# Optimization experiments

Measured on AMD Instinct MI355X. Metric: run time of the kernel, lower is better.

The kernel has to match this reference:

```python
import jax, jax.numpy as jnp
import numpy as np

N_NODES = 100000
N_EDGES = 1600000
DIM = 128


def setup_inputs() -> dict:
    key = jax.random.key(0)
    k1, k2, k3, k4 = jax.random.split(key, 4)
    x = jax.random.normal(k1, (N_NODES, DIM), dtype=jnp.float32)
    edge_index = jax.random.randint(k2, (2, N_EDGES), 0, N_NODES, dtype=jnp.int64)
    # PyG GCNConv params: Linear weight [out, in] (glorot) and bias [out] (zeros -> use small randn for a non-trivial grad path)
    W = jax.random.normal(k3, (DIM, DIM), dtype=jnp.float32) * (1.0 / np.sqrt(DIM))
    b = jax.random.normal(k4, (DIM,), dtype=jnp.float32) * 0.01
    return {"x": x, "edge_index": edge_index, "W": W, "b": b}


def reference(x, edge_index, W, b):
    # Faithful GCNConv: add self-loops, symmetric deg^-1/2 normalization,
    # linear transform, scatter-add aggregation, bias.
    N = x.shape[0]
    loop = jnp.arange(N, dtype=edge_index.dtype)
    src = jnp.concatenate([edge_index[0], loop])  # [E+N]
    dst = jnp.concatenate([edge_index[1], loop])  # [E+N]

    # degree (with self-loops) on destination nodes
    deg = jax.ops.segment_sum(jnp.ones_like(dst, dtype=x.dtype), dst, num_segments=N)
    dinv = jnp.where(deg > 0, jax.lax.rsqrt(deg), 0.0)
    norm = dinv[src] * dinv[dst]  # [E+N]

    x_lin = x @ W.T  # [N, dim] — PyG applies linear before propagate
    msg = x_lin[src] * norm[:, None]  # [E+N, dim] gather + scale
    out = jax.ops.segment_sum(msg, dst, num_segments=N)  # scatter-add aggregate
    return out + b
```

## Files before the change

kernel.cpp:

```cpp
#include <hip/hip_runtime.h>
#include <hip/hip_bf16.h>


#define DIM 128
#define BINSHIFT 9
#define BINSZ 512
#define MAXNB 256
#define WSTRIDE 136
#define SCAT_BLOCKS 256

typedef __attribute__((ext_vector_type(8))) short short8;
typedef __attribute__((ext_vector_type(4))) float f32x4;

__device__ inline unsigned short f2bf(float f) {
    unsigned u = __builtin_bit_cast(unsigned, f);
    return (unsigned short)((u + 0x7FFFu + ((u >> 16) & 1u)) >> 16);
}

__device__ inline void bf8_axpy(uint4 v, float s, float* acc) {
    acc[0] = fmaf(s, __builtin_bit_cast(float, v.x << 16), acc[0]);
    acc[1] = fmaf(s, __builtin_bit_cast(float, v.x & 0xFFFF0000u), acc[1]);
    acc[2] = fmaf(s, __builtin_bit_cast(float, v.y << 16), acc[2]);
    acc[3] = fmaf(s, __builtin_bit_cast(float, v.y & 0xFFFF0000u), acc[3]);
    acc[4] = fmaf(s, __builtin_bit_cast(float, v.z << 16), acc[4]);
    acc[5] = fmaf(s, __builtin_bit_cast(float, v.z & 0xFFFF0000u), acc[5]);
    acc[6] = fmaf(s, __builtin_bit_cast(float, v.w << 16), acc[6]);
    acc[7] = fmaf(s, __builtin_bit_cast(float, v.w & 0xFFFF0000u), acc[7]);
}


__global__ __launch_bounds__(256) void bin_hist(const int* __restrict__ dst, int E,
                                                int* __restrict__ hist, int nb) {
    __shared__ int lh[MAXNB];
    int t = threadIdx.x;
    lh[t] = 0;
    __syncthreads();
    int chunk = (E + gridDim.x - 1) / gridDim.x;
    int base = blockIdx.x * chunk, end = min(E, base + chunk);
    for (int i = base + t; i < end; i += 256)
        atomicAdd(&lh[dst[i] >> BINSHIFT], 1);
    __syncthreads();
    if (t < nb && lh[t]) atomicAdd(&hist[t], lh[t]);
}

__global__ __launch_bounds__(256) void bin_scan(const int* __restrict__ hist,
                                                int* __restrict__ binStart,
                                                int* __restrict__ binCursor,
                                                int* __restrict__ row_ptr,
                                                int nb, int N) {
    __shared__ int sa[MAXNB], sb[MAXNB];
    int t = threadIdx.x;
    sa[t] = (t < nb) ? hist[t] : 0;
    __syncthreads();
    int* src = sa; int* dstp = sb;
    for (int step = 1; step < MAXNB; step <<= 1) {
        int v = src[t];
        if (t >= step) v += src[t - step];
        dstp[t] = v;
        __syncthreads();
        int* tmp = src; src = dstp; dstp = tmp;
    }
    if (t < nb) {
        int excl = src[t] - hist[t];
        binStart[t] = excl;
        binCursor[t] = excl;
    }
    if (t == nb - 1) binStart[nb] = src[t];
    if (t == 0) row_ptr[N] = src[nb - 1];
}

__global__ __launch_bounds__(256) void csr_build(const int2* __restrict__ binned,
                                                 const int* __restrict__ binStart,
                                                 int* __restrict__ col,
                                                 int* __restrict__ row_ptr,
                                                 float* __restrict__ dinv, int N) {
    __shared__ int ldeg[BINSZ];
    __shared__ int sa[BINSZ], sb[BINSZ];
    __shared__ int lcur[BINSZ];
    int t = threadIdx.x, b = blockIdx.x;
    int s0 = binStart[b], s1 = binStart[b + 1];
    for (int i = t; i < BINSZ; i += 256) { ldeg[i] = 0; lcur[i] = 0; }
    __syncthreads();
    for (int i = s0 + t; i < s1; i += 256)
        atomicAdd(&ldeg[binned[i].y & (BINSZ - 1)], 1);
    __syncthreads();
    for (int i = t; i < BINSZ; i += 256) sa[i] = ldeg[i];
    __syncthreads();
    int* src = sa; int* dstp = sb;
    for (int step = 1; step < BINSZ; step <<= 1) {
        for (int i = t; i < BINSZ; i += 256) {
            int v = src[i];
            if (i >= step) v += src[i - step];
            dstp[i] = v;
        }
        __syncthreads();
        int* tmp = src; src = dstp; dstp = tmp;
    }
    for (int i = t; i < BINSZ; i += 256) dstp[i] = src[i] - ldeg[i];
    __syncthreads();
    for (int i = t; i < BINSZ; i += 256) {
        int n = (b << BINSHIFT) + i;
        if (n < N) {
            row_ptr[n] = s0 + dstp[i];
            dinv[n] = rsqrtf((float)(ldeg[i] + 1));
        }
    }
    for (int i = s0 + t; i < s1; i += 256) {
        int2 e = binned[i];
        int li = e.y & (BINSZ - 1);
        col[s0 + dstp[li] + atomicAdd(&lcur[li], 1)] = e.x;
    }
}


__global__ __launch_bounds__(256) void gemm_scatter(const float* __restrict__ x,
                                                    const float* __restrict__ W,
                                                    unsigned short* __restrict__ xlin, int N,
                                                    const int* __restrict__ ei, int E,
                                                    int* __restrict__ binCursor,
                                                    int2* __restrict__ binned, int nb) {
    __shared__ unsigned short wbf[DIM * WSTRIDE];
    __shared__ unsigned short obuf[4 * 16 * WSTRIDE];
    int t = threadIdx.x;

    if (blockIdx.x < SCAT_BLOCKS) {
        int* lh = (int*)wbf;
        int* lbase = lh + MAXNB;
        lh[t] = 0;
        __syncthreads();
        int chunk = (E + SCAT_BLOCKS - 1) / SCAT_BLOCKS;
        int base = blockIdx.x * chunk, end = min(E, base + chunk);
        for (int i = base + t; i < end; i += 256)
            atomicAdd(&lh[ei[E + i] >> BINSHIFT], 1);
        __syncthreads();
        if (t < nb) {
            int c = lh[t];
            lbase[t] = c ? atomicAdd(&binCursor[t], c) : 0;
            lh[t] = 0;
        }
        __syncthreads();
        for (int i = base + t; i < end; i += 256) {
            int s = ei[i], d = ei[E + i];
            int b = d >> BINSHIFT;
            int pos = lbase[b] + atomicAdd(&lh[b], 1);
            binned[pos] = make_int2(s, d);
        }
        return;
    }

    for (int it = 0; it < 16; ++it) {
        int f = it * 256 + t;
        int j = f >> 5;
        int kq = f & 31;
        float4 w4 = ((const float4*)W)[f];
        unsigned short* p = &wbf[j * WSTRIDE + kq * 4];
        p[0] = f2bf(w4.x); p[1] = f2bf(w4.y); p[2] = f2bf(w4.z); p[3] = f2bf(w4.w);
    }
    __syncthreads();

    int wid = t >> 6, lane = t & 63;
    int m = lane & 15, quad = lane >> 4;
    int row_base = (blockIdx.x - SCAT_BLOCKS) * 64 + wid * 16;

    f32x4 acc[8];
#pragma unroll
    for (int j = 0; j < 8; ++j) acc[j] = (f32x4){0.f, 0.f, 0.f, 0.f};

    int arow = row_base + m;
    if (arow >= N) arow = N - 1;
    const float* xr = x + (size_t)arow * DIM + quad * 8;

#pragma unroll
    for (int kc = 0; kc < 4; ++kc) {
        float4 a0 = *(const float4*)(xr + kc * 32);
        float4 a1 = *(const float4*)(xr + kc * 32 + 4);
        short8 af;
        af[0] = (short)f2bf(a0.x); af[1] = (short)f2bf(a0.y);
        af[2] = (short)f2bf(a0.z); af[3] = (short)f2bf(a0.w);
        af[4] = (short)f2bf(a1.x); af[5] = (short)f2bf(a1.y);
        af[6] = (short)f2bf(a1.z); af[7] = (short)f2bf(a1.w);
#pragma unroll
        for (int jt = 0; jt < 8; ++jt) {
            short8 bf = *(const short8*)&wbf[(jt * 16 + m) * WSTRIDE + kc * 32 + quad * 8];
            acc[jt] = __builtin_amdgcn_mfma_f32_16x16x32_bf16(af, bf, acc[jt], 0, 0, 0);
        }
    }

    unsigned short* ob = &obuf[wid * 16 * WSTRIDE];
#pragma unroll
    for (int jt = 0; jt < 8; ++jt)
#pragma unroll
        for (int r = 0; r < 4; ++r)
            ob[(quad * 4 + r) * WSTRIDE + jt * 16 + m] = f2bf(acc[jt][r]);
#pragma unroll
    for (int it = 0; it < 4; ++it) {
        int idx = it * 64 + lane;
        int r = idx >> 4;
        int cb = idx & 15;
        int grow = row_base + r;
        if (grow < N) {
            short8 v = *(const short8*)&ob[r * WSTRIDE + cb * 8];
            *(short8*)(xlin + (size_t)grow * DIM + cb * 8) = v;
        }
    }
}


__global__ __launch_bounds__(256) void aggregate(const unsigned short* __restrict__ xlin,
                                                 const int* __restrict__ col,
                                                 const int* __restrict__ row_ptr,
                                                 const float* __restrict__ dinv,
                                                 const float* __restrict__ bias,
                                                 float* __restrict__ out, int N) {
    int node = blockIdx.x * 16 + (threadIdx.x >> 4);
    int lane = threadIdx.x & 15;
    if (node >= N) return;

    float di = dinv[node];
    int r0 = row_ptr[node], r1 = row_ptr[node + 1];

    const uint4* xl = (const uint4*)xlin;
    float acc[8] = {};
    bf8_axpy(xl[(size_t)node * 16 + lane], di, acc);

    int i = r0;
    for (; i + 4 <= r1; i += 4) {
        int s0 = col[i], s1 = col[i + 1], s2 = col[i + 2], s3 = col[i + 3];
        float d0 = dinv[s0], d1 = dinv[s1], d2 = dinv[s2], d3 = dinv[s3];
        uint4 v0 = xl[(size_t)s0 * 16 + lane];
        uint4 v1 = xl[(size_t)s1 * 16 + lane];
        uint4 v2 = xl[(size_t)s2 * 16 + lane];
        uint4 v3 = xl[(size_t)s3 * 16 + lane];
        bf8_axpy(v0, d0, acc);
        bf8_axpy(v1, d1, acc);
        bf8_axpy(v2, d2, acc);
        bf8_axpy(v3, d3, acc);
    }
    for (; i < r1; ++i) {
        int s = col[i];
        bf8_axpy(xl[(size_t)s * 16 + lane], dinv[s], acc);
    }

    const float4* b4 = (const float4*)(bias + lane * 8);
    float4 bl = b4[0], bh = b4[1];
    float4 olo = make_float4(di * acc[0] + bl.x, di * acc[1] + bl.y,
                             di * acc[2] + bl.z, di * acc[3] + bl.w);
    float4 ohi = make_float4(di * acc[4] + bh.x, di * acc[5] + bh.y,
                             di * acc[6] + bh.z, di * acc[7] + bh.w);
    float4* op = (float4*)(out + (size_t)node * DIM + lane * 8);
    op[0] = olo;
    op[1] = ohi;
}


extern "C" void kernel_launch(void* const* d_in, const int* in_sizes, int n_in,
                              void* d_out, int out_size, void* d_ws, size_t ws_size,
                              hipStream_t stream) {
    const float* x    = (const float*)d_in[0];
    const int*   ei   = (const int*)d_in[1];
    const float* W    = (const float*)d_in[2];
    const float* bias = (const float*)d_in[3];
    float* out = (float*)d_out;

    const int N = in_sizes[0] / DIM;
    const int E = in_sizes[1] / 2;
    const int nb = (N + BINSZ - 1) >> BINSHIFT;

    char* ws = (char*)d_ws;
    size_t off = 0;
    auto alloc = [&](size_t bytes) { size_t o = off; off = (off + bytes + 255) & ~(size_t)255; return o; };
    unsigned short* xlin = (unsigned short*)(ws + alloc((size_t)N * DIM * 2));
    int2* binned   = (int2*) (ws + alloc((size_t)E * 8));
    int*  col      = (int*)  (ws + alloc((size_t)E * 4));
    int*  row_ptr  = (int*)  (ws + alloc((size_t)(N + 1) * 4));
    float* dinv    = (float*)(ws + alloc((size_t)N * 4));
    int*  hist     = (int*)  (ws + alloc(MAXNB * 4));
    int*  binStart = (int*)  (ws + alloc((MAXNB + 1) * 4));
    int*  binCursor= (int*)  (ws + alloc(MAXNB * 4));

    hipMemsetAsync(hist, 0, MAXNB * 4, stream);
    bin_hist<<<256, 256, 0, stream>>>(ei + E, E, hist, nb);
    bin_scan<<<1, MAXNB, 0, stream>>>(hist, binStart, binCursor, row_ptr, nb, N);
    gemm_scatter<<<SCAT_BLOCKS + (N + 63) / 64, 256, 0, stream>>>(
        x, W, xlin, N, ei, E, binCursor, binned, nb);
    csr_build<<<nb, 256, 0, stream>>>(binned, binStart, col, row_ptr, dinv, N);
    aggregate<<<(N + 15) / 16, 256, 0, stream>>>(xlin, col, row_ptr, dinv, bias, out, N);
}
```

Baseline: 232.5 us.

## Chunk xlin by feature columns and precompute bf16 W in histogram kernel

Stores xlin in feature-chunked layout (8 chunks of 16 columns, each N x 16) and makes aggregate blocks each handle one chunk for 128 nodes, two lanes per node. Consecutive blocks share a chunk group, so the gathered working set per chunk (about 3.2 MB) is meant to stay in L2/LDS-adjacent caches instead of random full-row gathers. Separately, the W-to-bf16 conversion moves into extra blocks of the histogram kernel, so GEMM blocks read W from global and no longer fill an LDS copy. The cost is rereading col/row_ptr/dinv eight times and shorter 32-byte gathers per edge.

```diff
diff --git a/kernel.cpp b/kernel.cpp
--- a/kernel.cpp
+++ b/kernel.cpp
@@ -8,9 +8,12 @@
 #define MAXNB 256
 #define WSTRIDE 136
 #define SCAT_BLOCKS 256
+#define HIST_BLOCKS 256
+#define NCHUNK 8
 
 typedef __attribute__((ext_vector_type(8))) short short8;
 typedef __attribute__((ext_vector_type(4))) float f32x4;
+typedef __attribute__((ext_vector_type(4))) unsigned short ushort4v;
 
 __device__ inline unsigned short f2bf(float f) {
     unsigned u = __builtin_bit_cast(unsigned, f);
@@ -28,14 +31,25 @@
     acc[7] = fmaf(s, __builtin_bit_cast(float, v.w & 0xFFFF0000u), acc[7]);
 }
 
-
-__global__ __launch_bounds__(256) void bin_hist(const int* __restrict__ dst, int E,
-                                                int* __restrict__ hist, int nb) {
+__global__ __launch_bounds__(256) void bin_hist_wconv(const int* __restrict__ dst, int E,
+                                                      int* __restrict__ hist, int nb,
+                                                      const float* __restrict__ W,
+                                                      unsigned short* __restrict__ wbf) {
+    int t = threadIdx.x;
+    if (blockIdx.x >= HIST_BLOCKS) {
+        int base = (blockIdx.x - HIST_BLOCKS) * 1024 + t * 4;
+#pragma unroll
+        for (int i = 0; i < 4; ++i) {
+            float4 w4 = ((const float4*)W)[base + i];
+            ushort4v o; o.x = f2bf(w4.x); o.y = f2bf(w4.y); o.z = f2bf(w4.z); o.w = f2bf(w4.w);
+            ((ushort4v*)wbf)[base + i] = o;
+        }
+        return;
+    }
     __shared__ int lh[MAXNB];
-    int t = threadIdx.x;
     lh[t] = 0;
     __syncthreads();
-    int chunk = (E + gridDim.x - 1) / gridDim.x;
+    int chunk = (E + HIST_BLOCKS - 1) / HIST_BLOCKS;
     int base = blockIdx.x * chunk, end = min(E, base + chunk);
     for (int i = base + t; i < end; i += 256)
         atomicAdd(&lh[dst[i] >> BINSHIFT], 1);
@@ -112,19 +126,17 @@
     }
 }
 
-
 __global__ __launch_bounds__(256) void gemm_scatter(const float* __restrict__ x,
-                                                    const float* __restrict__ W,
+                                                    const unsigned short* __restrict__ wbf,
                                                     unsigned short* __restrict__ xlin, int N,
                                                     const int* __restrict__ ei, int E,
                                                     int* __restrict__ binCursor,
                                                     int2* __restrict__ binned, int nb) {
-    __shared__ unsigned short wbf[DIM * WSTRIDE];
     __shared__ unsigned short obuf[4 * 16 * WSTRIDE];
     int t = threadIdx.x;
 
     if (blockIdx.x < SCAT_BLOCKS) {
-        int* lh = (int*)wbf;
+        int* lh = (int*)obuf;
         int* lbase = lh + MAXNB;
         lh[t] = 0;
         __syncthreads();
@@ -147,16 +159,6 @@
         }
         return;
     }
-
-    for (int it = 0; it < 16; ++it) {
-        int f = it * 256 + t;
-        int j = f >> 5;
-        int kq = f & 31;
-        float4 w4 = ((const float4*)W)[f];
-        unsigned short* p = &wbf[j * WSTRIDE + kq * 4];
-        p[0] = f2bf(w4.x); p[1] = f2bf(w4.y); p[2] = f2bf(w4.z); p[3] = f2bf(w4.w);
-    }
-    __syncthreads();
 
     int wid = t >> 6, lane = t & 63;
     int m = lane & 15, quad = lane >> 4;
@@ -181,7 +183,7 @@
         af[6] = (short)f2bf(a1.z); af[7] = (short)f2bf(a1.w);
 #pragma unroll
         for (int jt = 0; jt < 8; ++jt) {
-            short8 bf = *(const short8*)&wbf[(jt * 16 + m) * WSTRIDE + kc * 32 + quad * 8];
+            short8 bf = *(const short8*)&wbf[(jt * 16 + m) * DIM + kc * 32 + quad * 8];
             acc[jt] = __builtin_amdgcn_mfma_f32_16x16x32_bf16(af, bf, acc[jt], 0, 0, 0);
         }
     }
@@ -194,17 +196,15 @@
             ob[(quad * 4 + r) * WSTRIDE + jt * 16 + m] = f2bf(acc[jt][r]);
 #pragma unroll
     for (int it = 0; it < 4; ++it) {
-        int idx = it * 64 + lane;
-        int r = idx >> 4;
-        int cb = idx & 15;
+        int s = it * 64 + lane;
+        int c = s >> 5, r = (s >> 1) & 15, half = s & 1;
         int grow = row_base + r;
         if (grow < N) {
-            short8 v = *(const short8*)&ob[r * WSTRIDE + cb * 8];
-            *(short8*)(xlin + (size_t)grow * DIM + cb * 8) = v;
-        }
-    }
-}
-
+            short8 v = *(const short8*)&ob[r * WSTRIDE + c * 16 + half * 8];
+            *(short8*)(xlin + ((size_t)c * N + grow) * 16 + half * 8) = v;
+        }
+    }
+}
 
 __global__ __launch_bounds__(256) void aggregate(const unsigned short* __restrict__ xlin,
                                                  const int* __restrict__ col,
@@ -212,25 +212,27 @@
                                                  const float* __restrict__ dinv,
                                                  const float* __restrict__ bias,
                                                  float* __restrict__ out, int N) {
-    int node = blockIdx.x * 16 + (threadIdx.x >> 4);
-    int lane = threadIdx.x & 15;
+    int c = blockIdx.x & (NCHUNK - 1);
+    int g = blockIdx.x >> 3;
+    int node = g * 128 + (threadIdx.x >> 1);
+    int half = threadIdx.x & 1;
     if (node >= N) return;
 
     float di = dinv[node];
     int r0 = row_ptr[node], r1 = row_ptr[node + 1];
 
-    const uint4* xl = (const uint4*)xlin;
+    const uint4* base = (const uint4*)xlin + (size_t)c * N * 2;
     float acc[8] = {};
-    bf8_axpy(xl[(size_t)node * 16 + lane], di, acc);
+    bf8_axpy(base[(size_t)node * 2 + half], di, acc);
 
     int i = r0;
     for (; i + 4 <= r1; i += 4) {
         int s0 = col[i], s1 = col[i + 1], s2 = col[i + 2], s3 = col[i + 3];
         float d0 = dinv[s0], d1 = dinv[s1], d2 = dinv[s2], d3 = dinv[s3];
-        uint4 v0 = xl[(size_t)s0 * 16 + lane];
-        uint4 v1 = xl[(size_t)s1 * 16 + lane];
-        uint4 v2 = xl[(size_t)s2 * 16 + lane];
-        uint4 v3 = xl[(size_t)s3 * 16 + lane];
+        uint4 v0 = base[(size_t)s0 * 2 + half];
+        uint4 v1 = base[(size_t)s1 * 2 + half];
+        uint4 v2 = base[(size_t)s2 * 2 + half];
+        uint4 v3 = base[(size_t)s3 * 2 + half];
         bf8_axpy(v0, d0, acc);
         bf8_axpy(v1, d1, acc);
         bf8_axpy(v2, d2, acc);
@@ -238,16 +240,17 @@
     }
     for (; i < r1; ++i) {
         int s = col[i];
-        bf8_axpy(xl[(size_t)s * 16 + lane], dinv[s], acc);
-    }
-
-    const float4* b4 = (const float4*)(bias + lane * 8);
+        bf8_axpy(base[(size_t)s * 2 + half], dinv[s], acc);
+    }
+
+    int d0 = c * 16 + half * 8;
+    const float4* b4 = (const float4*)(bias + d0);
     float4 bl = b4[0], bh = b4[1];
     float4 olo = make_float4(di * acc[0] + bl.x, di * acc[1] + bl.y,
                              di * acc[2] + bl.z, di * acc[3] + bl.w);
     float4 ohi = make_float4(di * acc[4] + bh.x, di * acc[5] + bh.y,
                              di * acc[6] + bh.z, di * acc[7] + bh.w);
-    float4* op = (float4*)(out + (size_t)node * DIM + lane * 8);
+    float4* op = (float4*)(out + (size_t)node * DIM + d0);
     op[0] = olo;
     op[1] = ohi;
 }
@@ -277,12 +280,14 @@
     int*  hist     = (int*)  (ws + alloc(MAXNB * 4));
     int*  binStart = (int*)  (ws + alloc((MAXNB + 1) * 4));
     int*  binCursor= (int*)  (ws + alloc(MAXNB * 4));
+    unsigned short* wbf = (unsigned short*)(ws + alloc((size_t)DIM * DIM * 2));
 
     hipMemsetAsync(hist, 0, MAXNB * 4, stream);
-    bin_hist<<<256, 256, 0, stream>>>(ei + E, E, hist, nb);
+    bin_hist_wconv<<<HIST_BLOCKS + 4, 256, 0, stream>>>(ei + E, E, hist, nb, W, wbf);
     bin_scan<<<1, MAXNB, 0, stream>>>(hist, binStart, binCursor, row_ptr, nb, N);
     gemm_scatter<<<SCAT_BLOCKS + (N + 63) / 64, 256, 0, stream>>>(
-        x, W, xlin, N, ei, E, binCursor, binned, nb);
+        x, wbf, xlin, N, ei, E, binCursor, binned, nb);
     csr_build<<<nb, 256, 0, stream>>>(binned, binStart, col, row_ptr, dinv, N);
-    aggregate<<<(N + 15) / 16, 256, 0, stream>>>(xlin, col, row_ptr, dinv, bias, out, N);
-}
+    aggregate<<<((N + 127) / 128) * NCHUNK, 256, 0, stream>>>(
+        xlin, col, row_ptr, dinv, bias, out, N);
+}
```

Result: slower. 329.8 us (+41.8%).

## Use fixed-capacity bins to drop histogram pass and merge CSR build with GEMM

Applied to the files above, without the earlier changes.

The change replaces the global histogram and scan kernels with fixed-capacity per-bin slots (CAPB entries per bin), so edges can be scattered into bins without first knowing bin offsets. CSR construction then runs in the same launch as the bf16 MFMA GEMM, with W converted to bf16 once in global memory and read directly instead of staged in LDS. The aim is to cut kernel launches and a full pass over the edge list, and to overlap CSR building with the GEMM. In exchange it hardcodes NB=196 bins and a per-bin capacity that only holds for this graph size and degree distribution. The GEMM now reads unpadded W rows from global memory, and the aggregate tail loop issues redundant masked loads.

```diff
diff --git a/kernel.cpp b/kernel.cpp
--- a/kernel.cpp
+++ b/kernel.cpp
@@ -5,12 +5,15 @@
 #define DIM 128
 #define BINSHIFT 9
 #define BINSZ 512
+#define NB 196
 #define MAXNB 256
+#define CAPB 16384
 #define WSTRIDE 136
 #define SCAT_BLOCKS 256
 
 typedef __attribute__((ext_vector_type(8))) short short8;
 typedef __attribute__((ext_vector_type(4))) float f32x4;
+typedef __attribute__((ext_vector_type(4))) unsigned short ushort4v;
 
 __device__ inline unsigned short f2bf(float f) {
     unsigned u = __builtin_bit_cast(unsigned, f);
@@ -28,139 +31,99 @@
     acc[7] = fmaf(s, __builtin_bit_cast(float, v.w & 0xFFFF0000u), acc[7]);
 }
 
-
-__global__ __launch_bounds__(256) void bin_hist(const int* __restrict__ dst, int E,
-                                                int* __restrict__ hist, int nb) {
+__global__ __launch_bounds__(256) void scatter_wconv(const int* __restrict__ ei, int E,
+                                                     int* __restrict__ binCursor,
+                                                     int2* __restrict__ binned,
+                                                     const float* __restrict__ W,
+                                                     unsigned short* __restrict__ wbf) {
+    int t = threadIdx.x;
+    if (blockIdx.x >= SCAT_BLOCKS) {
+        int base = (blockIdx.x - SCAT_BLOCKS) * 1024 + t * 4;
+#pragma unroll
+        for (int i = 0; i < 4; ++i) {
+            float4 w4 = ((const float4*)W)[base + i];
+            ushort4v o; o.x = f2bf(w4.x); o.y = f2bf(w4.y); o.z = f2bf(w4.z); o.w = f2bf(w4.w);
+            ((ushort4v*)wbf)[base + i] = o;
+        }
+        return;
+    }
     __shared__ int lh[MAXNB];
-    int t = threadIdx.x;
+    __shared__ int lbase[MAXNB];
     lh[t] = 0;
     __syncthreads();
-    int chunk = (E + gridDim.x - 1) / gridDim.x;
+    int chunk = (E + SCAT_BLOCKS - 1) / SCAT_BLOCKS;
     int base = blockIdx.x * chunk, end = min(E, base + chunk);
     for (int i = base + t; i < end; i += 256)
-        atomicAdd(&lh[dst[i] >> BINSHIFT], 1);
+        atomicAdd(&lh[ei[E + i] >> BINSHIFT], 1);
     __syncthreads();
-    if (t < nb && lh[t]) atomicAdd(&hist[t], lh[t]);
-}
-
-__global__ __launch_bounds__(256) void bin_scan(const int* __restrict__ hist,
-                                                int* __restrict__ binStart,
-                                                int* __restrict__ binCursor,
-                                                int* __restrict__ row_ptr,
-                                                int nb, int N) {
-    __shared__ int sa[MAXNB], sb[MAXNB];
+    if (t < NB) {
+        int c = lh[t];
+        lbase[t] = c ? atomicAdd(&binCursor[t], c) : 0;
+        lh[t] = 0;
+    }
+    __syncthreads();
+    for (int i = base + t; i < end; i += 256) {
+        int s = ei[i], d = ei[E + i];
+        int b = d >> BINSHIFT;
+        int pos = b * CAPB + lbase[b] + atomicAdd(&lh[b], 1);
+        binned[pos] = make_int2(s, d);
+    }
+}
+
+
+__global__ __launch_bounds__(256) void csr_gemm(const int2* __restrict__ binned,
+                                                const int* __restrict__ binCursor,
+                                                int* __restrict__ col,
+                                                int2* __restrict__ rowinfo,
+                                                float* __restrict__ dinv,
+                                                const float* __restrict__ x,
+                                                const unsigned short* __restrict__ wbf,
+                                                unsigned short* __restrict__ xlin, int N) {
+    __shared__ unsigned short obuf[4 * 16 * WSTRIDE];
+    __shared__ int ldeg[BINSZ], sa[BINSZ], sb[BINSZ], lcur[BINSZ];
     int t = threadIdx.x;
-    sa[t] = (t < nb) ? hist[t] : 0;
-    __syncthreads();
-    int* src = sa; int* dstp = sb;
-    for (int step = 1; step < MAXNB; step <<= 1) {
-        int v = src[t];
-        if (t >= step) v += src[t - step];
-        dstp[t] = v;
-        __syncthreads();
-        int* tmp = src; src = dstp; dstp = tmp;
-    }
-    if (t < nb) {
-        int excl = src[t] - hist[t];
-        binStart[t] = excl;
-        binCursor[t] = excl;
-    }
-    if (t == nb - 1) binStart[nb] = src[t];
-    if (t == 0) row_ptr[N] = src[nb - 1];
-}
-
-__global__ __launch_bounds__(256) void csr_build(const int2* __restrict__ binned,
-                                                 const int* __restrict__ binStart,
-                                                 int* __restrict__ col,
-                                                 int* __restrict__ row_ptr,
-                                                 float* __restrict__ dinv, int N) {
-    __shared__ int ldeg[BINSZ];
-    __shared__ int sa[BINSZ], sb[BINSZ];
-    __shared__ int lcur[BINSZ];
-    int t = threadIdx.x, b = blockIdx.x;
-    int s0 = binStart[b], s1 = binStart[b + 1];
-    for (int i = t; i < BINSZ; i += 256) { ldeg[i] = 0; lcur[i] = 0; }
-    __syncthreads();
-    for (int i = s0 + t; i < s1; i += 256)
-        atomicAdd(&ldeg[binned[i].y & (BINSZ - 1)], 1);
-    __syncthreads();
-    for (int i = t; i < BINSZ; i += 256) sa[i] = ldeg[i];
-    __syncthreads();
-    int* src = sa; int* dstp = sb;
-    for (int step = 1; step < BINSZ; step <<= 1) {
+
+    if (blockIdx.x < NB) {
+        int b = blockIdx.x;
+        int s0 = b * CAPB;
+        int s1 = s0 + binCursor[b];
+        for (int i = t; i < BINSZ; i += 256) { ldeg[i] = 0; lcur[i] = 0; }
+        __syncthreads();
+        for (int i = s0 + t; i < s1; i += 256)
+            atomicAdd(&ldeg[binned[i].y & (BINSZ - 1)], 1);
+        __syncthreads();
+        for (int i = t; i < BINSZ; i += 256) sa[i] = ldeg[i];
+        __syncthreads();
+        int* src = sa; int* dstp = sb;
+        for (int step = 1; step < BINSZ; step <<= 1) {
+            for (int i = t; i < BINSZ; i += 256) {
+                int v = src[i];
+                if (i >= step) v += src[i - step];
+                dstp[i] = v;
+            }
+            __syncthreads();
+            int* tmp = src; src = dstp; dstp = tmp;
+        }
+        for (int i = t; i < BINSZ; i += 256) dstp[i] = src[i] - ldeg[i];
+        __syncthreads();
         for (int i = t; i < BINSZ; i += 256) {
-            int v = src[i];
-            if (i >= step) v += src[i - step];
-            dstp[i] = v;
-        }
-        __syncthreads();
-        int* tmp = src; src = dstp; dstp = tmp;
-    }
-    for (int i = t; i < BINSZ; i += 256) dstp[i] = src[i] - ldeg[i];
-    __syncthreads();
-    for (int i = t; i < BINSZ; i += 256) {
-        int n = (b << BINSHIFT) + i;
-        if (n < N) {
-            row_ptr[n] = s0 + dstp[i];
-            dinv[n] = rsqrtf((float)(ldeg[i] + 1));
-        }
-    }
-    for (int i = s0 + t; i < s1; i += 256) {
-        int2 e = binned[i];
-        int li = e.y & (BINSZ - 1);
-        col[s0 + dstp[li] + atomicAdd(&lcur[li], 1)] = e.x;
-    }
-}
-
-
-__global__ __launch_bounds__(256) void gemm_scatter(const float* __restrict__ x,
-                                                    const float* __restrict__ W,
-                                                    unsigned short* __restrict__ xlin, int N,
-                                                    const int* __restrict__ ei, int E,
-                                                    int* __restrict__ binCursor,
-                                                    int2* __restrict__ binned, int nb) {
-    __shared__ unsigned short wbf[DIM * WSTRIDE];
-    __shared__ unsigned short obuf[4 * 16 * WSTRIDE];
-    int t = threadIdx.x;
-
-    if (blockIdx.x < SCAT_BLOCKS) {
-        int* lh = (int*)wbf;
-        int* lbase = lh + MAXNB;
-        lh[t] = 0;
-        __syncthreads();
-        int chunk = (E + SCAT_BLOCKS - 1) / SCAT_BLOCKS;
-        int base = blockIdx.x * chunk, end = min(E, base + chunk);
-        for (int i = base + t; i < end; i += 256)
-            atomicAdd(&lh[ei[E + i] >> BINSHIFT], 1);
-        __syncthreads();
-        if (t < nb) {
-            int c = lh[t];
-            lbase[t] = c ? atomicAdd(&binCursor[t], c) : 0;
-            lh[t] = 0;
-        }
-        __syncthreads();
-        for (int i = base + t; i < end; i += 256) {
-            int s = ei[i], d = ei[E + i];
-            int b = d >> BINSHIFT;
-            int pos = lbase[b] + atomicAdd(&lh[b], 1);
-            binned[pos] = make_int2(s, d);
+            int n = (b << BINSHIFT) + i;
+            if (n < N) {
+                rowinfo[n] = make_int2(s0 + dstp[i], ldeg[i]);
+                dinv[n] = rsqrtf((float)(ldeg[i] + 1));
+            }
+        }
+        for (int i = s0 + t; i < s1; i += 256) {
+            int2 e = binned[i];
+            int li = e.y & (BINSZ - 1);
+            col[s0 + dstp[li] + atomicAdd(&lcur[li], 1)] = e.x;
         }
         return;
     }
-
-    for (int it = 0; it < 16; ++it) {
-        int f = it * 256 + t;
-        int j = f >> 5;
-        int kq = f & 31;
-        float4 w4 = ((const float4*)W)[f];
-        unsigned short* p = &wbf[j * WSTRIDE + kq * 4];
-        p[0] = f2bf(w4.x); p[1] = f2bf(w4.y); p[2] = f2bf(w4.z); p[3] = f2bf(w4.w);
-    }
-    __syncthreads();
 
     int wid = t >> 6, lane = t & 63;
     int m = lane & 15, quad = lane >> 4;
-    int row_base = (blockIdx.x - SCAT_BLOCKS) * 64 + wid * 16;
+    int row_base = (blockIdx.x - NB) * 64 + wid * 16;
 
     f32x4 acc[8];
 #pragma unroll
@@ -181,7 +144,7 @@
         af[6] = (short)f2bf(a1.z); af[7] = (short)f2bf(a1.w);
 #pragma unroll
         for (int jt = 0; jt < 8; ++jt) {
-            short8 bf = *(const short8*)&wbf[(jt * 16 + m) * WSTRIDE + kc * 32 + quad * 8];
+            short8 bf = *(const short8*)&wbf[(jt * 16 + m) * DIM + kc * 32 + quad * 8];
             acc[jt] = __builtin_amdgcn_mfma_f32_16x16x32_bf16(af, bf, acc[jt], 0, 0, 0);
         }
     }
@@ -208,7 +171,7 @@
 
 __global__ __launch_bounds__(256) void aggregate(const unsigned short* __restrict__ xlin,
                                                  const int* __restrict__ col,
-                                                 const int* __restrict__ row_ptr,
+                                                 const int2* __restrict__ rowinfo,
                                                  const float* __restrict__ dinv,
                                                  const float* __restrict__ bias,
                                                  float* __restrict__ out, int N) {
@@ -217,16 +180,23 @@
     if (node >= N) return;
 
     float di = dinv[node];
-    int r0 = row_ptr[node], r1 = row_ptr[node + 1];
+    int2 ri = rowinfo[node];
+    int r0 = ri.x, r1 = ri.x + ri.y;
 
     const uint4* xl = (const uint4*)xlin;
     float acc[8] = {};
     bf8_axpy(xl[(size_t)node * 16 + lane], di, acc);
 
-    int i = r0;
-    for (; i + 4 <= r1; i += 4) {
-        int s0 = col[i], s1 = col[i + 1], s2 = col[i + 2], s3 = col[i + 3];
-        float d0 = dinv[s0], d1 = dinv[s1], d2 = dinv[s2], d3 = dinv[s3];
+    for (int i = r0; i < r1; i += 4) {
+        int rem = r1 - i;
+        int s0 = col[i];
+        int s1 = col[rem > 1 ? i + 1 : i];
+        int s2 = col[rem > 2 ? i + 2 : i];
+        int s3 = col[rem > 3 ? i + 3 : i];
+        float d0 = dinv[s0];
+        float d1 = rem > 1 ? dinv[s1] : 0.f;
+        float d2 = rem > 2 ? dinv[s2] : 0.f;
+        float d3 = rem > 3 ? dinv[s3] : 0.f;
         uint4 v0 = xl[(size_t)s0 * 16 + lane];
         uint4 v1 = xl[(size_t)s1 * 16 + lane];
         uint4 v2 = xl[(size_t)s2 * 16 + lane];
@@ -235,10 +205,6 @@
         bf8_axpy(v1, d1, acc);
         bf8_axpy(v2, d2, acc);
         bf8_axpy(v3, d3, acc);
-    }
-    for (; i < r1; ++i) {
-        int s = col[i];
-        bf8_axpy(xl[(size_t)s * 16 + lane], dinv[s], acc);
     }
 
     const float4* b4 = (const float4*)(bias + lane * 8);
@@ -264,25 +230,21 @@
 
     const int N = in_sizes[0] / DIM;
     const int E = in_sizes[1] / 2;
-    const int nb = (N + BINSZ - 1) >> BINSHIFT;
 
     char* ws = (char*)d_ws;
     size_t off = 0;
     auto alloc = [&](size_t bytes) { size_t o = off; off = (off + bytes + 255) & ~(size_t)255; return o; };
     unsigned short* xlin = (unsigned short*)(ws + alloc((size_t)N * DIM * 2));
-    int2* binned   = (int2*) (ws + alloc((size_t)E * 8));
-    int*  col      = (int*)  (ws + alloc((size_t)E * 4));
-    int*  row_ptr  = (int*)  (ws + alloc((size_t)(N + 1) * 4));
+    int2* binned   = (int2*) (ws + alloc((size_t)NB * CAPB * 8));
+    int*  col      = (int*)  (ws + alloc((size_t)NB * CAPB * 4));
+    int2* rowinfo  = (int2*) (ws + alloc((size_t)N * 8));
     float* dinv    = (float*)(ws + alloc((size_t)N * 4));
-    int*  hist     = (int*)  (ws + alloc(MAXNB * 4));
-    int*  binStart = (int*)  (ws + alloc((MAXNB + 1) * 4));
     int*  binCursor= (int*)  (ws + alloc(MAXNB * 4));
-
-    hipMemsetAsync(hist, 0, MAXNB * 4, stream);
-    bin_hist<<<256, 256, 0, stream>>>(ei + E, E, hist, nb);
-    bin_scan<<<1, MAXNB, 0, stream>>>(hist, binStart, binCursor, row_ptr, nb, N);
-    gemm_scatter<<<SCAT_BLOCKS + (N + 63) / 64, 256, 0, stream>>>(
-        x, W, xlin, N, ei, E, binCursor, binned, nb);
-    csr_build<<<nb, 256, 0, stream>>>(binned, binStart, col, row_ptr, dinv, N);
-    aggregate<<<(N + 15) / 16, 256, 0, stream>>>(xlin, col, row_ptr, dinv, bias, out, N);
-}
+    unsigned short* wbf = (unsigned short*)(ws + alloc((size_t)DIM * DIM * 2));
+
+    hipMemsetAsync(binCursor, 0, MAXNB * 4, stream);
+    scatter_wconv<<<SCAT_BLOCKS + 4, 256, 0, stream>>>(ei, E, binCursor, binned, W, wbf);
+    csr_gemm<<<NB + (N + 63) / 64, 256, 0, stream>>>(
+        binned, binCursor, col, rowinfo, dinv, x, wbf, xlin, N);
+    aggregate<<<(N + 15) / 16, 256, 0, stream>>>(xlin, col, rowinfo, dinv, bias, out, N);
+}
```

After: 232.0 us. About the same (-0.2%).
